# Kernel tuning notes

Measured on AMD Instinct MI355X. Metric: run time of the kernel, lower is better.

Reference implementation:

```python
import jax, jax.numpy as jnp
import numpy as np

B, D, N = 8, 512, 4096
HEADS, DH = 8, 64
HID = HEADS * DH  # 512
SCALE = DH ** -0.5


def setup_inputs() -> dict:
    key = jax.random.key(0)
    k0, k1, k2, k3 = jax.random.split(key, 4)
    x = jax.random.normal(k0, (B, D, N), dtype=jnp.float32)
    w_qkv = jax.random.normal(k1, (3 * HID, D), dtype=jnp.float32) * 0.02
    w_out = jax.random.normal(k2, (D, HID), dtype=jnp.float32) * 0.02
    b_out = jax.random.normal(k3, (D,), dtype=jnp.float32) * 0.02
    g = jnp.ones((1, D, 1), dtype=jnp.float32)
    return {"x": x, "w_qkv": w_qkv, "w_out": w_out, "b_out": b_out, "g": g}


def reference(x, w_qkv, w_out, b_out, g):
    # 1x1 Conv1d (no bias) == channel matmul: [b, 3*HID, n]
    qkv = jnp.einsum('od,bdn->bon', w_qkv, x)
    q, k, v = jnp.split(qkv, 3, axis=1)
    # b (h c) n -> b h c n
    q = q.reshape(B, HEADS, DH, N)
    k = k.reshape(B, HEADS, DH, N)
    v = v.reshape(B, HEADS, DH, N)
    q = jax.nn.softmax(q, axis=2) * SCALE  # softmax over feature dim d
    k = jax.nn.softmax(k, axis=3)          # softmax over sequence dim n
    context = jnp.einsum('bhdn,bhen->bhde', k, v)   # [b,h,d,e]
    out = jnp.einsum('bhde,bhdn->bhen', context, q)  # [b,h,e,n]
    out = out.reshape(B, HID, N)
    # 1x1 Conv1d with bias
    y = jnp.einsum('oh,bhn->bon', w_out, out) + b_out[None, :, None]
    # RMSNorm: F.normalize(y, dim=1) * g * sqrt(D)
    norm = jnp.sqrt(jnp.sum(y * y, axis=1, keepdims=True))
    y = y / jnp.maximum(norm, 1e-12) * g * jnp.asarray(D, y.dtype) ** 0.5
    return y
```

## Files before the change

### kernel.cpp

```cpp
#include <hip/hip_runtime.h>
#include <math.h>

#define B 8
#define D 512
#define N 4096
#define HEADS 8
#define DH 64
#define HID 512
#define O3 1536
#define KDIM 512
#define SCALE 0.125f
#define SQRT_D 22.62741699796952f

typedef __attribute__((ext_vector_type(4))) float f32x4;
typedef __attribute__((ext_vector_type(8))) short bf16x8;

static __device__ __forceinline__ unsigned short f2bf(float f) {
    unsigned int u = __float_as_uint(f);
    unsigned int r = (u + 0x7fffu + ((u >> 16) & 1u)) >> 16;
    return (unsigned short)r;
}

static __device__ __forceinline__ float bf2f(unsigned short u) {
    return __uint_as_float((unsigned int)u << 16);
}

static __device__ __forceinline__ void gload_lds16(const void* g, void* l) {
    __builtin_amdgcn_global_load_lds(
        (const __attribute__((address_space(1))) unsigned int*)g,
        (__attribute__((address_space(3))) unsigned int*)l, 16, 0, 0);
}

__global__ __launch_bounds__(256) void cvt_w(const float* __restrict__ w,
                                             unsigned short* __restrict__ wb) {
    int i = (blockIdx.x * 256 + threadIdx.x) * 4;
    float4 v = *(const float4*)(w + i);
    __align__(8) unsigned short o[4] = {f2bf(v.x), f2bf(v.y), f2bf(v.z), f2bf(v.w)};
    *(uint2*)(wb + i) = *(const uint2*)o;
}

__global__ __launch_bounds__(256) void transpose_x(const float* __restrict__ x,
                                                   unsigned short* __restrict__ xT) {
    __shared__ float tile[64][65];
    const int n0 = blockIdx.x * 64, d0 = blockIdx.y * 64, b = blockIdx.z;
    const float* xb = x + (size_t)b * D * N;
    unsigned short* xTb = xT + (size_t)b * N * KDIM;
    const int t = threadIdx.x;
    const int r = t >> 4, c4 = (t & 15) * 4;
#pragma unroll
    for (int i = 0; i < 4; ++i) {
        int row = r + i * 16;
        float4 v = *(const float4*)(xb + (size_t)(d0 + row) * N + n0 + c4);
        tile[row][c4 + 0] = v.x;
        tile[row][c4 + 1] = v.y;
        tile[row][c4 + 2] = v.z;
        tile[row][c4 + 3] = v.w;
    }
    __syncthreads();
#pragma unroll
    for (int pass = 0; pass < 2; ++pass) {
        int orow = (t >> 3) + pass * 32;
        int oc = (t & 7) * 8;
        __align__(16) unsigned short o[8];
#pragma unroll
        for (int e = 0; e < 8; ++e) o[e] = f2bf(tile[oc + e][orow]);
        *(uint4*)(xTb + (size_t)(n0 + orow) * KDIM + d0 + oc) = *(const uint4*)o;
    }
}

#define STAGE_AB(A_PTR, BT_PTR, BUFOFF, KOFF)                                      \
    _Pragma("unroll") for (int i = 0; i < 4; ++i)                                  \
        gload_lds16(A_PTR + (size_t)(row0 + prow[i]) * KDIM + (KOFF) + coff[i],    \
                    (char*)As + (BUFOFF) + i * 4096 + t * 16);                     \
    _Pragma("unroll") for (int i = 0; i < 4; ++i)                                  \
        gload_lds16(BT_PTR + (size_t)(col0 + prow[i]) * KDIM + (KOFF) + coff[i],   \
                    (char*)Bs + (BUFOFF) + i * 4096 + t * 16);

#define GEMM_CORE_DB(A_PTR, BT_PTR, ACC)                                           \
    __shared__ __align__(16) unsigned short As[2 * 128 * 64];                      \
    __shared__ __align__(16) unsigned short Bs[2 * 128 * 64];                      \
    const int t = threadIdx.x;                                                     \
    const int lane = t & 63;                                                       \
    const int wid = t >> 6;                                                        \
    const int wm = wid >> 1, wn = wid & 1;                                         \
    int prow[4], coff[4];                                                          \
    _Pragma("unroll") for (int i = 0; i < 4; ++i) {                                \
        int p = i * 4096 + t * 16;                                                 \
        int pr = p >> 7;                                                           \
        int pc = (p >> 4) & 7;                                                     \
        prow[i] = pr;                                                              \
        coff[i] = (pc ^ (pr & 7)) * 8;                                             \
    }                                                                              \
    int aoff[4][2], boff[4][2];                                                    \
    _Pragma("unroll") for (int m = 0; m < 4; ++m) {                                \
        int arow = wm * 64 + m * 16 + (lane & 15);                                 \
        int brow = wn * 64 + m * 16 + (lane & 15);                                 \
        _Pragma("unroll") for (int s = 0; s < 2; ++s) {                            \
            int chunk = s * 4 + (lane >> 4);                                       \
            aoff[m][s] = arow * 128 + ((chunk ^ (arow & 7)) << 4);                 \
            boff[m][s] = brow * 128 + ((chunk ^ (brow & 7)) << 4);                 \
        }                                                                          \
    }                                                                              \
    f32x4 ACC[4][4] = {};                                                          \
    { STAGE_AB(A_PTR, BT_PTR, 0, 0) }                                              \
    for (int kt = 0; kt < 8; ++kt) {                                               \
        if (kt < 7) {                                                              \
            STAGE_AB(A_PTR, BT_PTR, ((kt + 1) & 1) * 16384, (kt + 1) * 64)         \
            asm volatile("s_waitcnt vmcnt(8)" ::: "memory");                       \
        } else {                                                                   \
            asm volatile("s_waitcnt vmcnt(0)" ::: "memory");                       \
        }                                                                          \
        __builtin_amdgcn_s_barrier();                                              \
        const int bo = (kt & 1) * 16384;                                           \
        bf16x8 af[4][2], bfr[4][2];                                                \
        _Pragma("unroll") for (int m = 0; m < 4; ++m)                              \
            _Pragma("unroll") for (int s = 0; s < 2; ++s) {                        \
                af[m][s] = *(const bf16x8*)((const char*)As + bo + aoff[m][s]);    \
                bfr[m][s] = *(const bf16x8*)((const char*)Bs + bo + boff[m][s]);   \
            }                                                                      \
        asm volatile("s_waitcnt lgkmcnt(0)" ::: "memory");                         \
        __builtin_amdgcn_sched_barrier(0);                                         \
        __builtin_amdgcn_s_barrier();                                              \
        _Pragma("unroll") for (int s = 0; s < 2; ++s)                              \
            _Pragma("unroll") for (int m = 0; m < 4; ++m)                          \
                _Pragma("unroll") for (int n = 0; n < 4; ++n)                      \
                    ACC[m][n] = __builtin_amdgcn_mfma_f32_16x16x32_bf16(           \
                        af[m][s], bfr[n][s], ACC[m][n], 0, 0, 0);                  \
    }

__global__ __launch_bounds__(256) void gemm_qkv(const unsigned short* __restrict__ Aw,
                                                const unsigned short* __restrict__ BTall,
                                                unsigned short* __restrict__ qT,
                                                unsigned short* __restrict__ kvall) {
    const int b = blockIdx.z;
    const unsigned short* A = Aw;
    const unsigned short* BT = BTall + (size_t)b * N * KDIM;
    const int row0 = blockIdx.y * 128;
    const int col0 = blockIdx.x * 128;
    GEMM_CORE_DB(A, BT, acc)

    if (blockIdx.y < 4) {
        const int h = blockIdx.y * 2 + wm;
        const int g = lane >> 4;
#pragma unroll
        for (int nf = 0; nf < 4; ++nf) {
            float mx = -1e30f;
#pragma unroll
            for (int m = 0; m < 4; ++m)
#pragma unroll
                for (int r = 0; r < 4; ++r) mx = fmaxf(mx, acc[m][nf][r]);
            mx = fmaxf(mx, __shfl_xor(mx, 16));
            mx = fmaxf(mx, __shfl_xor(mx, 32));
            float e[16];
            float s = 0.f;
#pragma unroll
            for (int m = 0; m < 4; ++m)
#pragma unroll
                for (int r = 0; r < 4; ++r) {
                    e[m * 4 + r] = __expf(acc[m][nf][r] - mx);
                    s += e[m * 4 + r];
                }
            s += __shfl_xor(s, 16);
            s += __shfl_xor(s, 32);
            float rs = SCALE / s;
            int n = col0 + wn * 64 + nf * 16 + (lane & 15);
            unsigned short* dst = qT + ((size_t)b * N + n) * KDIM + h * 64 + g * 4;
#pragma unroll
            for (int m = 0; m < 4; ++m) {
                __align__(8) unsigned short o4[4] = {
                    f2bf(e[m * 4 + 0] * rs), f2bf(e[m * 4 + 1] * rs),
                    f2bf(e[m * 4 + 2] * rs), f2bf(e[m * 4 + 3] * rs)};
                *(uint2*)(dst + m * 16) = *(const uint2*)o4;
            }
        }
    } else {
        unsigned short* C = kvall + (size_t)b * 1024 * N;
        const int rbase = row0 - 512;
#pragma unroll
        for (int m = 0; m < 4; ++m) {
            int row_b = rbase + wm * 64 + m * 16 + (lane >> 4) * 4;
#pragma unroll
            for (int n = 0; n < 4; ++n) {
                int col = col0 + wn * 64 + n * 16 + (lane & 15);
#pragma unroll
                for (int r = 0; r < 4; ++r)
                    C[(size_t)(row_b + r) * N + col] = f2bf(acc[m][n][r]);
            }
        }
    }
}

__global__ __launch_bounds__(256) void context_mfma3(const unsigned short* __restrict__ kvb,
                                                     float* __restrict__ ctx,
                                                     float* __restrict__ ksum) {
    const int ch = blockIdx.x, h = blockIdx.y, b = blockIdx.z;
    const int K0 = ch * 512;
    const unsigned short* kbase = kvb + ((size_t)b * 1024 + h * DH) * (size_t)N + K0;
    const unsigned short* vbase = kvb + ((size_t)b * 1024 + 512 + h * DH) * (size_t)N + K0;

    __shared__ __align__(16) unsigned short Ks[64 * 64];
    __shared__ __align__(16) unsigned short Vs[64 * 64];

    const int t = threadIdx.x;
    const int lane = t & 63;
    const int wv = t >> 6;

    const int kr = t >> 2;
    const int kc = (t & 3) * 16;
    const int kchunk0 = kc >> 3;
    const int kdst0 = kr * 128 + (((kchunk0 + 0) ^ (kr & 7)) << 4);
    const int kdst1 = kr * 128 + (((kchunk0 + 1) ^ (kr & 7)) << 4);

    int vrow[2], vcoff[2];
#pragma unroll
    for (int i = 0; i < 2; ++i) {
        int p = i * 4096 + t * 16;
        int pr = p >> 7;
        int pc = (p >> 4) & 7;
        vrow[i] = pr;
        vcoff[i] = (pc ^ (pr & 7)) * 8;
    }

    const int ar = wv * 16 + (lane & 15);
    int aoff[2], boff[4][2];
#pragma unroll
    for (int s = 0; s < 2; ++s) {
        int chunk = s * 4 + (lane >> 4);
        aoff[s] = ar * 128 + ((chunk ^ (ar & 7)) << 4);
#pragma unroll
        for (int nf = 0; nf < 4; ++nf) {
            int br = nf * 16 + (lane & 15);
            boff[nf][s] = br * 128 + ((chunk ^ (br & 7)) << 4);
        }
    }

    bf16x8 ones;
#pragma unroll
    for (int j = 0; j < 8; ++j) ones[j] = (short)0x3F80;

    f32x4 acc[4] = {};
    f32x4 accs = {};

    for (int k0 = 0; k0 < 512; k0 += 64) {
#pragma unroll
        for (int i = 0; i < 2; ++i)
            gload_lds16(vbase + (size_t)vrow[i] * N + k0 + vcoff[i],
                        (char*)Vs + i * 4096 + t * 16);
        __align__(16) unsigned short raw[16];
        *(uint4*)raw = *(const uint4*)(kbase + (size_t)kr * N + k0 + kc);
        *(uint4*)(raw + 8) = *(const uint4*)(kbase + (size_t)kr * N + k0 + kc + 8);
        __align__(16) unsigned short o[16];
#pragma unroll
        for (int j = 0; j < 16; ++j) o[j] = f2bf(__expf(bf2f(raw[j])));
        *(uint4*)((char*)Ks + kdst0) = *(const uint4*)o;
        *(uint4*)((char*)Ks + kdst1) = *(const uint4*)(o + 8);
        __syncthreads();

        bf16x8 av[2], bv[4][2];
#pragma unroll
        for (int s = 0; s < 2; ++s) {
            av[s] = *(const bf16x8*)((const char*)Ks + aoff[s]);
#pragma unroll
            for (int nf = 0; nf < 4; ++nf)
                bv[nf][s] = *(const bf16x8*)((const char*)Vs + boff[nf][s]);
        }
#pragma unroll
        for (int s = 0; s < 2; ++s) {
#pragma unroll
            for (int nf = 0; nf < 4; ++nf)
                acc[nf] = __builtin_amdgcn_mfma_f32_16x16x32_bf16(av[s], bv[nf][s], acc[nf], 0, 0, 0);
            accs = __builtin_amdgcn_mfma_f32_16x16x32_bf16(av[s], ones, accs, 0, 0, 0);
        }
        __syncthreads();
    }

    float* cbase = ctx + ((size_t)(b * HEADS + h)) * DH * DH;
    const int drow = wv * 16 + (lane >> 4) * 4;
#pragma unroll
    for (int nf = 0; nf < 4; ++nf) {
        int e = nf * 16 + (lane & 15);
#pragma unroll
        for (int rr = 0; rr < 4; ++rr)
            atomicAdd(&cbase[(drow + rr) * DH + e], acc[nf][rr]);
    }
    if ((lane & 15) == 0) {
#pragma unroll
        for (int rr = 0; rr < 4; ++rr)
            atomicAdd(&ksum[b * 512 + h * DH + drow + rr], accs[rr]);
    }
}

__global__ __launch_bounds__(256) void fold_wout3(const float* __restrict__ w_out,
                                                  const float* __restrict__ ctx,
                                                  const float* __restrict__ ksum,
                                                  unsigned short* __restrict__ w2) {
    const int ot = blockIdx.x, h = blockIdx.y, b = blockIdx.z;
    __shared__ __align__(16) unsigned short As[128 * 64];
    __shared__ __align__(16) unsigned short Bs[64 * 64];
    const int t = threadIdx.x;
    const int lane = t & 63;
    const int wv = t >> 6;

#pragma unroll
    for (int i = 0; i < 8; ++i) {
        int lin = t + i * 256;
        int r = lin >> 4;
        int c4 = (lin & 15) * 4;
        float4 v = *(const float4*)(w_out + (size_t)(ot * 128 + r) * HID + h * 64 + c4);
        __align__(8) unsigned short o4[4] = {f2bf(v.x), f2bf(v.y), f2bf(v.z), f2bf(v.w)};
        int chunk = c4 >> 3;
        int off = (c4 & 7) * 2;
        *(uint2*)((char*)As + r * 128 + ((chunk ^ (r & 7)) << 4) + off) = *(const uint2*)o4;
    }
    const float* cb = ctx + ((size_t)(b * HEADS + h)) * DH * DH;
    const float* ks = ksum + b * 512 + h * 64;
#pragma unroll
    for (int i = 0; i < 4; ++i) {
        int lin = t + i * 256;
        int r = lin >> 4;
        int c4 = (lin & 15) * 4;
        float inv = 1.0f / ks[r];
        float4 v = *(const float4*)(cb + (size_t)r * DH + c4);
        __align__(8) unsigned short o4[4] = {f2bf(v.x * inv), f2bf(v.y * inv),
                                             f2bf(v.z * inv), f2bf(v.w * inv)};
        int chunk = c4 >> 3;
        int off = (c4 & 7) * 2;
        *(uint2*)((char*)Bs + r * 128 + ((chunk ^ (r & 7)) << 4) + off) = *(const uint2*)o4;
    }
    __syncthreads();

    f32x4 acc[2][4] = {};
#pragma unroll
    for (int s = 0; s < 2; ++s) {
        int chunk = s * 4 + (lane >> 4);
        bf16x8 bf[4];
#pragma unroll
        for (int nf = 0; nf < 4; ++nf) {
            int brow = nf * 16 + (lane & 15);
            bf[nf] = *(const bf16x8*)((const char*)Bs + brow * 128 + ((chunk ^ (brow & 7)) << 4));
        }
#pragma unroll
        for (int mm = 0; mm < 2; ++mm) {
            int arow = (wv * 2 + mm) * 16 + (lane & 15);
            bf16x8 a = *(const bf16x8*)((const char*)As + arow * 128 + ((chunk ^ (arow & 7)) << 4));
#pragma unroll
            for (int nf = 0; nf < 4; ++nf)
                acc[mm][nf] = __builtin_amdgcn_mfma_f32_16x16x32_bf16(a, bf[nf], acc[mm][nf], 0, 0, 0);
        }
    }

#pragma unroll
    for (int mm = 0; mm < 2; ++mm) {
        int o_base = ot * 128 + (wv * 2 + mm) * 16 + (lane >> 4) * 4;
#pragma unroll
        for (int nf = 0; nf < 4; ++nf) {
            int d = nf * 16 + (lane & 15);
#pragma unroll
            for (int rr = 0; rr < 4; ++rr)
                w2[((size_t)(b * D) + o_base + rr) * D + h * 64 + d] = f2bf(acc[mm][nf][rr]);
        }
    }
}

__global__ __launch_bounds__(256) void gemm_y(const unsigned short* __restrict__ w2all,
                                              const unsigned short* __restrict__ qTall,
                                              const float* __restrict__ bias,
                                              float* __restrict__ yall,
                                              float* __restrict__ colsum) {
    const int b = blockIdx.z;
    const unsigned short* A = w2all + (size_t)b * D * D;
    const unsigned short* BT = qTall + (size_t)b * N * KDIM;
    float* y = yall + (size_t)b * D * N;
    const int row0 = blockIdx.y * 128;
    const int col0 = blockIdx.x * 128;
    GEMM_CORE_DB(A, BT, acc)

    float csum[4] = {0.f, 0.f, 0.f, 0.f};
#pragma unroll
    for (int m = 0; m < 4; ++m) {
        int row_b = row0 + wm * 64 + m * 16 + (lane >> 4) * 4;
#pragma unroll
        for (int r = 0; r < 4; ++r) {
            float bv = bias[row_b + r];
#pragma unroll
            for (int n = 0; n < 4; ++n) {
                int col = col0 + wn * 64 + n * 16 + (lane & 15);
                float e = acc[m][n][r] + bv;
                y[(size_t)(row_b + r) * N + col] = e;
                csum[n] += e * e;
            }
        }
    }
#pragma unroll
    for (int n = 0; n < 4; ++n) {
        csum[n] += __shfl_xor(csum[n], 16);
        csum[n] += __shfl_xor(csum[n], 32);
    }
    if (lane < 16) {
#pragma unroll
        for (int n = 0; n < 4; ++n) {
            int col = col0 + wn * 64 + n * 16 + lane;
            atomicAdd(&colsum[b * N + col], csum[n]);
        }
    }
}

__global__ __launch_bounds__(256) void colprep(float* __restrict__ cs) {
    int i = blockIdx.x * 256 + threadIdx.x;
    float v = cs[i];
    cs[i] = SQRT_D / fmaxf(sqrtf(v), 1e-12f);
}

__global__ __launch_bounds__(256) void rmsnorm4(float4* __restrict__ y,
                                                const float4* __restrict__ rinv,
                                                const float* __restrict__ g) {
    const size_t total = (size_t)B * D * N / 4;
    for (size_t i = blockIdx.x * 256 + threadIdx.x; i < total; i += 524288) {
        int b = (int)(i >> 19);
        int rem = (int)(i & 524287);
        int o = rem >> 10;
        int n4 = rem & 1023;
        float4 v = y[i];
        float4 rv = rinv[b * 1024 + n4];
        float go = g[o];
        v.x *= rv.x * go;
        v.y *= rv.y * go;
        v.z *= rv.z * go;
        v.w *= rv.w * go;
        y[i] = v;
    }
}

extern "C" void kernel_launch(void* const* d_in, const int* in_sizes, int n_in,
                              void* d_out, int out_size, void* d_ws, size_t ws_size,
                              hipStream_t stream) {
    const float* x = (const float*)d_in[0];
    const float* w_qkv = (const float*)d_in[1];
    const float* w_out = (const float*)d_in[2];
    const float* b_out = (const float*)d_in[3];
    const float* g = (const float*)d_in[4];
    float* out = (float*)d_out;

    unsigned short* kvb = (unsigned short*)d_ws;
    float* ctx = (float*)(kvb + (size_t)B * 1024 * N);
    float* ksum = ctx + (size_t)B * HEADS * DH * DH;
    float* colsum = ksum + B * 512;
    unsigned short* w2 = (unsigned short*)(colsum + B * N);
    unsigned short* wqb = w2 + (size_t)B * D * D;
    unsigned short* xT = wqb + (size_t)O3 * KDIM;
    unsigned short* qT = xT + (size_t)B * N * KDIM;

    hipMemsetAsync(ctx, 0,
                   ((size_t)B * HEADS * DH * DH + B * 512 + B * N) * sizeof(float), stream);

    cvt_w<<<dim3(O3 * KDIM / 1024), 256, 0, stream>>>(w_qkv, wqb);
    transpose_x<<<dim3(N / 64, D / 64, B), 256, 0, stream>>>(x, xT);

    gemm_qkv<<<dim3(N / 128, O3 / 128, B), 256, 0, stream>>>(wqb, xT, qT, kvb);

    context_mfma3<<<dim3(8, HEADS, B), 256, 0, stream>>>(kvb, ctx, ksum);
    fold_wout3<<<dim3(4, HEADS, B), 256, 0, stream>>>(w_out, ctx, ksum, w2);

    gemm_y<<<dim3(N / 128, D / 128, B), 256, 0, stream>>>(w2, qT, b_out, out, colsum);

    colprep<<<dim3(B * N / 256), 256, 0, stream>>>(colsum);
    rmsnorm4<<<dim3(2048), 256, 0, stream>>>((float4*)out, (const float4*)colsum, g);
}
```

Measured before the change: 166.1 us.

## Load GEMM A fragments directly from global into registers, double-buffered

The A operand (weights) is no longer staged through shared memory. Each lane now loads its MFMA fragments straight from global memory into two register buffers, one prefetched a step ahead, while B keeps its LDS double buffer. This removes half of the LDS traffic and LDS footprint and some ds_read work per k-step. The cost is uncoalesced 16-byte global loads per lane with duplication across waves, more VGPRs for the double-buffered fragments, and a fully unrolled k loop.

```diff
diff --git a/kernel.cpp b/kernel.cpp
--- a/kernel.cpp
+++ b/kernel.cpp
@@ -68,16 +68,17 @@
     }
 }
 
-#define STAGE_AB(A_PTR, BT_PTR, BUFOFF, KOFF)                                      \
-    _Pragma("unroll") for (int i = 0; i < 4; ++i)                                  \
-        gload_lds16(A_PTR + (size_t)(row0 + prow[i]) * KDIM + (KOFF) + coff[i],    \
-                    (char*)As + (BUFOFF) + i * 4096 + t * 16);                     \
+#define STAGE_B(BT_PTR, BUFOFF, KOFF)                                              \
     _Pragma("unroll") for (int i = 0; i < 4; ++i)                                  \
         gload_lds16(BT_PTR + (size_t)(col0 + prow[i]) * KDIM + (KOFF) + coff[i],   \
                     (char*)Bs + (BUFOFF) + i * 4096 + t * 16);
 
-#define GEMM_CORE_DB(A_PTR, BT_PTR, ACC)                                           \
-    __shared__ __align__(16) unsigned short As[2 * 128 * 64];                      \
+#define LOAD_A(DST, KOFF)                                                          \
+    _Pragma("unroll") for (int m = 0; m < 4; ++m)                                  \
+        _Pragma("unroll") for (int s = 0; s < 2; ++s)                              \
+            DST[m][s] = *(const bf16x8*)(arow_[m] + (KOFF) + s * 32);
+
+#define GEMM_CORE_AG(A_PTR, BT_PTR, ACC)                                           \
     __shared__ __align__(16) unsigned short Bs[2 * 128 * 64];                      \
     const int t = threadIdx.x;                                                     \
     const int lane = t & 63;                                                       \
@@ -91,33 +92,40 @@
         prow[i] = pr;                                                              \
         coff[i] = (pc ^ (pr & 7)) * 8;                                             \
     }                                                                              \
-    int aoff[4][2], boff[4][2];                                                    \
-    _Pragma("unroll") for (int m = 0; m < 4; ++m) {                                \
-        int arow = wm * 64 + m * 16 + (lane & 15);                                 \
-        int brow = wn * 64 + m * 16 + (lane & 15);                                 \
+    int boff[4][2];                                                                \
+    _Pragma("unroll") for (int n = 0; n < 4; ++n) {                                \
+        int brow = wn * 64 + n * 16 + (lane & 15);                                 \
         _Pragma("unroll") for (int s = 0; s < 2; ++s) {                            \
             int chunk = s * 4 + (lane >> 4);                                       \
-            aoff[m][s] = arow * 128 + ((chunk ^ (arow & 7)) << 4);                 \
-            boff[m][s] = brow * 128 + ((chunk ^ (brow & 7)) << 4);                 \
+            boff[n][s] = brow * 128 + ((chunk ^ (brow & 7)) << 4);                 \
         }                                                                          \
     }                                                                              \
+    const unsigned short* arow_[4];                                                \
+    _Pragma("unroll") for (int m = 0; m < 4; ++m)                                  \
+        arow_[m] = A_PTR + (size_t)(row0 + wm * 64 + m * 16 + (lane & 15)) * KDIM  \
+                   + 8 * (lane >> 4);                                              \
     f32x4 ACC[4][4] = {};                                                          \
-    { STAGE_AB(A_PTR, BT_PTR, 0, 0) }                                              \
-    for (int kt = 0; kt < 8; ++kt) {                                               \
+    bf16x8 afA[4][2], afB[4][2];                                                   \
+    { STAGE_B(BT_PTR, 0, 0) }                                                      \
+    LOAD_A(afA, 0)                                                                 \
+    _Pragma("unroll") for (int kt = 0; kt < 8; ++kt) {                             \
         if (kt < 7) {                                                              \
-            STAGE_AB(A_PTR, BT_PTR, ((kt + 1) & 1) * 16384, (kt + 1) * 64)         \
-            asm volatile("s_waitcnt vmcnt(8)" ::: "memory");                       \
+            STAGE_B(BT_PTR, ((kt + 1) & 1) * 16384, (kt + 1) * 64)                 \
+            if ((kt & 1) == 0) {                                                   \
+                LOAD_A(afB, (kt + 1) * 64)                                         \
+            } else {                                                               \
+                LOAD_A(afA, (kt + 1) * 64)                                         \
+            }                                                                      \
+            asm volatile("s_waitcnt vmcnt(12)" ::: "memory");                      \
         } else {                                                                   \
             asm volatile("s_waitcnt vmcnt(0)" ::: "memory");                       \
         }                                                                          \
         __builtin_amdgcn_s_barrier();                                              \
         const int bo = (kt & 1) * 16384;                                           \
-        bf16x8 af[4][2], bfr[4][2];                                                \
-        _Pragma("unroll") for (int m = 0; m < 4; ++m)                              \
-            _Pragma("unroll") for (int s = 0; s < 2; ++s) {                        \
-                af[m][s] = *(const bf16x8*)((const char*)As + bo + aoff[m][s]);    \
-                bfr[m][s] = *(const bf16x8*)((const char*)Bs + bo + boff[m][s]);   \
-            }                                                                      \
+        bf16x8 bfr[4][2];                                                          \
+        _Pragma("unroll") for (int n = 0; n < 4; ++n)                              \
+            _Pragma("unroll") for (int s = 0; s < 2; ++s)                          \
+                bfr[n][s] = *(const bf16x8*)((const char*)Bs + bo + boff[n][s]);   \
         asm volatile("s_waitcnt lgkmcnt(0)" ::: "memory");                         \
         __builtin_amdgcn_sched_barrier(0);                                         \
         __builtin_amdgcn_s_barrier();                                              \
@@ -125,7 +133,7 @@
             _Pragma("unroll") for (int m = 0; m < 4; ++m)                          \
                 _Pragma("unroll") for (int n = 0; n < 4; ++n)                      \
                     ACC[m][n] = __builtin_amdgcn_mfma_f32_16x16x32_bf16(           \
-                        af[m][s], bfr[n][s], ACC[m][n], 0, 0, 0);                  \
+                        ((kt & 1) ? afB : afA)[m][s], bfr[n][s], ACC[m][n], 0, 0, 0); \
     }
 
 __global__ __launch_bounds__(256) void gemm_qkv(const unsigned short* __restrict__ Aw,
@@ -137,7 +145,7 @@
     const unsigned short* BT = BTall + (size_t)b * N * KDIM;
     const int row0 = blockIdx.y * 128;
     const int col0 = blockIdx.x * 128;
-    GEMM_CORE_DB(A, BT, acc)
+    GEMM_CORE_AG(A, BT, acc)
 
     if (blockIdx.y < 4) {
         const int h = blockIdx.y * 2 + wm;
@@ -373,7 +381,7 @@
     float* y = yall + (size_t)b * D * N;
     const int row0 = blockIdx.y * 128;
     const int col0 = blockIdx.x * 128;
-    GEMM_CORE_DB(A, BT, acc)
+    GEMM_CORE_AG(A, BT, acc)
 
     float csum[4] = {0.f, 0.f, 0.f, 0.f};
 #pragma unroll
```

Result: slower. 233.8 us (+40.7%).

## Use 256x256 GEMM tiles with 8 waves and interleaved staged loads

Applied to the files above, without the earlier changes.

Both projection GEMMs move from 128x128 tiles with 4 waves to 256x256 tiles with 8 waves and 128KB of double-buffered LDS. The main loop now interleaves next-tile global-to-LDS loads with four phases of fragment loads and MFMAs, and raises wave priority around the MFMA blocks. The larger tiles are meant to improve operand reuse and hide memory latency. In exchange there are fewer blocks (grid of 16x2x8 for gemm_y), heavier register and LDS pressure that may limit occupancy, and reworked epilogue indexing.

```diff
diff --git a/kernel.cpp b/kernel.cpp
--- a/kernel.cpp
+++ b/kernel.cpp
@@ -68,123 +68,135 @@
     }
 }
 
-#define STAGE_AB(A_PTR, BT_PTR, BUFOFF, KOFF)                                      \
-    _Pragma("unroll") for (int i = 0; i < 4; ++i)                                  \
-        gload_lds16(A_PTR + (size_t)(row0 + prow[i]) * KDIM + (KOFF) + coff[i],    \
-                    (char*)As + (BUFOFF) + i * 4096 + t * 16);                     \
-    _Pragma("unroll") for (int i = 0; i < 4; ++i)                                  \
-        gload_lds16(BT_PTR + (size_t)(col0 + prow[i]) * KDIM + (KOFF) + coff[i],   \
-                    (char*)Bs + (BUFOFF) + i * 4096 + t * 16);
-
-#define GEMM_CORE_DB(A_PTR, BT_PTR, ACC)                                           \
-    __shared__ __align__(16) unsigned short As[2 * 128 * 64];                      \
-    __shared__ __align__(16) unsigned short Bs[2 * 128 * 64];                      \
+#define STAGE_H(PTR, REGION, TILE0, KT, H)                                         \
+    _Pragma("unroll") for (int sub = 0; sub < 2; ++sub)                            \
+        gload_lds16(PTR + (size_t)((TILE0) + (H) * 128 + spr[sub]) * KDIM          \
+                        + (KT) * 64 + scoff[sub],                                  \
+                    lds + (REGION) + ((KT) & 1) * 32768 + (H) * 16384              \
+                        + sub * 8192 + t * 16);
+
+#define PHASE_A(MG, KS)                                                            \
+    _Pragma("unroll") for (int j = 0; j < 4; ++j)                                  \
+        afr[j] = *(const bf16x8*)(lds + rbuf + arb + ((MG) * 4 + j) * 2048 + xa[KS]);
+
+#define PHASE_B(KS)                                                                \
+    _Pragma("unroll") for (int nf = 0; nf < 4; ++nf)                               \
+        bfr[nf] = *(const bf16x8*)(lds + 65536 + rbuf + brb + nf * 2048 + xa[KS]);
+
+#define PHASE_MMA(MG)                                                              \
+    asm volatile("s_waitcnt lgkmcnt(0)" ::: "memory");                             \
+    __builtin_amdgcn_sched_barrier(0);                                             \
+    __builtin_amdgcn_s_setprio(1);                                                 \
+    _Pragma("unroll") for (int j = 0; j < 4; ++j)                                  \
+        _Pragma("unroll") for (int nf = 0; nf < 4; ++nf)                           \
+            acc[(MG) * 4 + j][nf] = __builtin_amdgcn_mfma_f32_16x16x32_bf16(       \
+                afr[j], bfr[nf], acc[(MG) * 4 + j][nf], 0, 0, 0);                  \
+    __builtin_amdgcn_s_setprio(0);
+
+#define GEMM256_CORE(A_PTR, BT_PTR)                                                \
+    __shared__ __align__(16) char lds[131072];                                     \
     const int t = threadIdx.x;                                                     \
     const int lane = t & 63;                                                       \
     const int wid = t >> 6;                                                        \
-    const int wm = wid >> 1, wn = wid & 1;                                         \
-    int prow[4], coff[4];                                                          \
-    _Pragma("unroll") for (int i = 0; i < 4; ++i) {                                \
-        int p = i * 4096 + t * 16;                                                 \
-        int pr = p >> 7;                                                           \
-        int pc = (p >> 4) & 7;                                                     \
-        prow[i] = pr;                                                              \
-        coff[i] = (pc ^ (pr & 7)) * 8;                                             \
+    const int wm = wid >> 2, wn = wid & 3;                                         \
+    int spr[2], scoff[2];                                                          \
+    _Pragma("unroll") for (int sub = 0; sub < 2; ++sub) {                          \
+        int p = sub * 8192 + t * 16;                                               \
+        spr[sub] = p >> 7;                                                         \
+        int spc = (p >> 4) & 7;                                                    \
+        scoff[sub] = (spc ^ (spr[sub] & 7)) * 8;                                   \
     }                                                                              \
-    int aoff[4][2], boff[4][2];                                                    \
-    _Pragma("unroll") for (int m = 0; m < 4; ++m) {                                \
-        int arow = wm * 64 + m * 16 + (lane & 15);                                 \
-        int brow = wn * 64 + m * 16 + (lane & 15);                                 \
-        _Pragma("unroll") for (int s = 0; s < 2; ++s) {                            \
-            int chunk = s * 4 + (lane >> 4);                                       \
-            aoff[m][s] = arow * 128 + ((chunk ^ (arow & 7)) << 4);                 \
-            boff[m][s] = brow * 128 + ((chunk ^ (brow & 7)) << 4);                 \
-        }                                                                          \
-    }                                                                              \
-    f32x4 ACC[4][4] = {};                                                          \
-    { STAGE_AB(A_PTR, BT_PTR, 0, 0) }                                              \
+    int xa[2];                                                                     \
+    _Pragma("unroll") for (int ks = 0; ks < 2; ++ks)                               \
+        xa[ks] = ((ks * 4 + (lane >> 4)) ^ (lane & 7)) << 4;                       \
+    const int arb = (wm * 128 + (lane & 15)) * 128;                                \
+    const int brb = (wn * 64 + (lane & 15)) * 128;                                 \
+    f32x4 acc[8][4] = {};                                                          \
+    bf16x8 afr[4], bfr[4];                                                         \
+    STAGE_H(A_PTR, 0, row0, 0, 0)                                                  \
+    STAGE_H(A_PTR, 0, row0, 0, 1)                                                  \
+    STAGE_H(BT_PTR, 65536, col0, 0, 0)                                             \
+    STAGE_H(BT_PTR, 65536, col0, 0, 1)                                             \
     for (int kt = 0; kt < 8; ++kt) {                                               \
+        const int rbuf = (kt & 1) * 32768;                                         \
+        __builtin_amdgcn_s_barrier();                                              \
         if (kt < 7) {                                                              \
-            STAGE_AB(A_PTR, BT_PTR, ((kt + 1) & 1) * 16384, (kt + 1) * 64)         \
-            asm volatile("s_waitcnt vmcnt(8)" ::: "memory");                       \
+            STAGE_H(A_PTR, 0, row0, kt + 1, 0)                                     \
+            asm volatile("s_waitcnt vmcnt(2)" ::: "memory");                       \
         } else {                                                                   \
             asm volatile("s_waitcnt vmcnt(0)" ::: "memory");                       \
         }                                                                          \
         __builtin_amdgcn_s_barrier();                                              \
-        const int bo = (kt & 1) * 16384;                                           \
-        bf16x8 af[4][2], bfr[4][2];                                                \
-        _Pragma("unroll") for (int m = 0; m < 4; ++m)                              \
-            _Pragma("unroll") for (int s = 0; s < 2; ++s) {                        \
-                af[m][s] = *(const bf16x8*)((const char*)As + bo + aoff[m][s]);    \
-                bfr[m][s] = *(const bf16x8*)((const char*)Bs + bo + boff[m][s]);   \
-            }                                                                      \
-        asm volatile("s_waitcnt lgkmcnt(0)" ::: "memory");                         \
         __builtin_amdgcn_sched_barrier(0);                                         \
-        __builtin_amdgcn_s_barrier();                                              \
-        _Pragma("unroll") for (int s = 0; s < 2; ++s)                              \
-            _Pragma("unroll") for (int m = 0; m < 4; ++m)                          \
-                _Pragma("unroll") for (int n = 0; n < 4; ++n)                      \
-                    ACC[m][n] = __builtin_amdgcn_mfma_f32_16x16x32_bf16(           \
-                        af[m][s], bfr[n][s], ACC[m][n], 0, 0, 0);                  \
-    }
-
-__global__ __launch_bounds__(256) void gemm_qkv(const unsigned short* __restrict__ Aw,
-                                                const unsigned short* __restrict__ BTall,
-                                                unsigned short* __restrict__ qT,
-                                                unsigned short* __restrict__ kvall) {
+        PHASE_A(0, 0) PHASE_B(0) PHASE_MMA(0)                                      \
+        if (kt < 7) { STAGE_H(A_PTR, 0, row0, kt + 1, 1) }                         \
+        PHASE_A(1, 0) PHASE_MMA(1)                                                 \
+        if (kt < 7) { STAGE_H(BT_PTR, 65536, col0, kt + 1, 0) }                    \
+        PHASE_A(0, 1) PHASE_B(1) PHASE_MMA(0)                                      \
+        if (kt < 7) { STAGE_H(BT_PTR, 65536, col0, kt + 1, 1) }                    \
+        PHASE_A(1, 1) PHASE_MMA(1)                                                 \
+    }
+
+__global__ __launch_bounds__(512, 2) void gemm_qkv(const unsigned short* __restrict__ Aw,
+                                                   const unsigned short* __restrict__ BTall,
+                                                   unsigned short* __restrict__ qT,
+                                                   unsigned short* __restrict__ kvall) {
     const int b = blockIdx.z;
     const unsigned short* A = Aw;
     const unsigned short* BT = BTall + (size_t)b * N * KDIM;
-    const int row0 = blockIdx.y * 128;
-    const int col0 = blockIdx.x * 128;
-    GEMM_CORE_DB(A, BT, acc)
-
-    if (blockIdx.y < 4) {
-        const int h = blockIdx.y * 2 + wm;
-        const int g = lane >> 4;
-#pragma unroll
-        for (int nf = 0; nf < 4; ++nf) {
-            float mx = -1e30f;
-#pragma unroll
-            for (int m = 0; m < 4; ++m)
-#pragma unroll
-                for (int r = 0; r < 4; ++r) mx = fmaxf(mx, acc[m][nf][r]);
-            mx = fmaxf(mx, __shfl_xor(mx, 16));
-            mx = fmaxf(mx, __shfl_xor(mx, 32));
-            float e[16];
-            float s = 0.f;
-#pragma unroll
-            for (int m = 0; m < 4; ++m)
-#pragma unroll
-                for (int r = 0; r < 4; ++r) {
-                    e[m * 4 + r] = __expf(acc[m][nf][r] - mx);
-                    s += e[m * 4 + r];
+    const int row0 = blockIdx.y * 256;
+    const int col0 = blockIdx.x * 256;
+    GEMM256_CORE(A, BT)
+
+    const int g = lane >> 4;
+    if (blockIdx.y < 2) {
+#pragma unroll
+        for (int g2 = 0; g2 < 2; ++g2) {
+            const int h = blockIdx.y * 4 + wm * 2 + g2;
+#pragma unroll
+            for (int nf = 0; nf < 4; ++nf) {
+                float mx = -1e30f;
+#pragma unroll
+                for (int j = 0; j < 4; ++j)
+#pragma unroll
+                    for (int r = 0; r < 4; ++r) mx = fmaxf(mx, acc[g2 * 4 + j][nf][r]);
+                mx = fmaxf(mx, __shfl_xor(mx, 16));
+                mx = fmaxf(mx, __shfl_xor(mx, 32));
+                float e[16];
+                float s = 0.f;
+#pragma unroll
+                for (int j = 0; j < 4; ++j)
+#pragma unroll
+                    for (int r = 0; r < 4; ++r) {
+                        e[j * 4 + r] = __expf(acc[g2 * 4 + j][nf][r] - mx);
+                        s += e[j * 4 + r];
+                    }
+                s += __shfl_xor(s, 16);
+                s += __shfl_xor(s, 32);
+                float rs = SCALE / s;
+                int n = col0 + wn * 64 + nf * 16 + (lane & 15);
+                unsigned short* dst = qT + ((size_t)b * N + n) * KDIM + h * 64 + g * 4;
+#pragma unroll
+                for (int j = 0; j < 4; ++j) {
+                    __align__(8) unsigned short o4[4] = {
+                        f2bf(e[j * 4 + 0] * rs), f2bf(e[j * 4 + 1] * rs),
+                        f2bf(e[j * 4 + 2] * rs), f2bf(e[j * 4 + 3] * rs)};
+                    *(uint2*)(dst + j * 16) = *(const uint2*)o4;
                 }
-            s += __shfl_xor(s, 16);
-            s += __shfl_xor(s, 32);
-            float rs = SCALE / s;
-            int n = col0 + wn * 64 + nf * 16 + (lane & 15);
-            unsigned short* dst = qT + ((size_t)b * N + n) * KDIM + h * 64 + g * 4;
-#pragma unroll
-            for (int m = 0; m < 4; ++m) {
-                __align__(8) unsigned short o4[4] = {
-                    f2bf(e[m * 4 + 0] * rs), f2bf(e[m * 4 + 1] * rs),
-                    f2bf(e[m * 4 + 2] * rs), f2bf(e[m * 4 + 3] * rs)};
-                *(uint2*)(dst + m * 16) = *(const uint2*)o4;
             }
         }
     } else {
         unsigned short* C = kvall + (size_t)b * 1024 * N;
-        const int rbase = row0 - 512;
-#pragma unroll
-        for (int m = 0; m < 4; ++m) {
-            int row_b = rbase + wm * 64 + m * 16 + (lane >> 4) * 4;
-#pragma unroll
-            for (int n = 0; n < 4; ++n) {
-                int col = col0 + wn * 64 + n * 16 + (lane & 15);
+        const int rbase = row0 - 512 + wm * 128;
+#pragma unroll
+        for (int mf = 0; mf < 8; ++mf) {
+            int row_b = rbase + mf * 16 + g * 4;
+#pragma unroll
+            for (int nf = 0; nf < 4; ++nf) {
+                int col = col0 + wn * 64 + nf * 16 + (lane & 15);
 #pragma unroll
                 for (int r = 0; r < 4; ++r)
-                    C[(size_t)(row_b + r) * N + col] = f2bf(acc[m][n][r]);
+                    C[(size_t)(row_b + r) * N + col] = f2bf(acc[mf][nf][r]);
             }
         }
     }
@@ -362,45 +374,46 @@
     }
 }
 
-__global__ __launch_bounds__(256) void gemm_y(const unsigned short* __restrict__ w2all,
-                                              const unsigned short* __restrict__ qTall,
-                                              const float* __restrict__ bias,
-                                              float* __restrict__ yall,
-                                              float* __restrict__ colsum) {
+__global__ __launch_bounds__(512, 2) void gemm_y(const unsigned short* __restrict__ w2all,
+                                                 const unsigned short* __restrict__ qTall,
+                                                 const float* __restrict__ bias,
+                                                 float* __restrict__ yall,
+                                                 float* __restrict__ colsum) {
     const int b = blockIdx.z;
     const unsigned short* A = w2all + (size_t)b * D * D;
     const unsigned short* BT = qTall + (size_t)b * N * KDIM;
     float* y = yall + (size_t)b * D * N;
-    const int row0 = blockIdx.y * 128;
-    const int col0 = blockIdx.x * 128;
-    GEMM_CORE_DB(A, BT, acc)
-
+    const int row0 = blockIdx.y * 256;
+    const int col0 = blockIdx.x * 256;
+    GEMM256_CORE(A, BT)
+
+    const int g = lane >> 4;
     float csum[4] = {0.f, 0.f, 0.f, 0.f};
 #pragma unroll
-    for (int m = 0; m < 4; ++m) {
-        int row_b = row0 + wm * 64 + m * 16 + (lane >> 4) * 4;
+    for (int mf = 0; mf < 8; ++mf) {
+        int row_b = row0 + wm * 128 + mf * 16 + g * 4;
 #pragma unroll
         for (int r = 0; r < 4; ++r) {
             float bv = bias[row_b + r];
 #pragma unroll
-            for (int n = 0; n < 4; ++n) {
-                int col = col0 + wn * 64 + n * 16 + (lane & 15);
-                float e = acc[m][n][r] + bv;
+            for (int nf = 0; nf < 4; ++nf) {
+                int col = col0 + wn * 64 + nf * 16 + (lane & 15);
+                float e = acc[mf][nf][r] + bv;
                 y[(size_t)(row_b + r) * N + col] = e;
-                csum[n] += e * e;
+                csum[nf] += e * e;
             }
         }
     }
 #pragma unroll
-    for (int n = 0; n < 4; ++n) {
-        csum[n] += __shfl_xor(csum[n], 16);
-        csum[n] += __shfl_xor(csum[n], 32);
-    }
-    if (lane < 16) {
-#pragma unroll
-        for (int n = 0; n < 4; ++n) {
-            int col = col0 + wn * 64 + n * 16 + lane;
-            atomicAdd(&colsum[b * N + col], csum[n]);
+    for (int nf = 0; nf < 4; ++nf) {
+        csum[nf] += __shfl_xor(csum[nf], 16);
+        csum[nf] += __shfl_xor(csum[nf], 32);
+    }
+    if ((lane & 48) == 0) {
+#pragma unroll
+        for (int nf = 0; nf < 4; ++nf) {
+            int col = col0 + wn * 64 + nf * 16 + (lane & 15);
+            atomicAdd(&colsum[b * N + col], csum[nf]);
         }
     }
 }
@@ -456,12 +469,12 @@
     cvt_w<<<dim3(O3 * KDIM / 1024), 256, 0, stream>>>(w_qkv, wqb);
     transpose_x<<<dim3(N / 64, D / 64, B), 256, 0, stream>>>(x, xT);
 
-    gemm_qkv<<<dim3(N / 128, O3 / 128, B), 256, 0, stream>>>(wqb, xT, qT, kvb);
+    gemm_qkv<<<dim3(N / 256, O3 / 256, B), 512, 0, stream>>>(wqb, xT, qT, kvb);
 
     context_mfma3<<<dim3(8, HEADS, B), 256, 0, stream>>>(kvb, ctx, ksum);
     fold_wout3<<<dim3(4, HEADS, B), 256, 0, stream>>>(w_out, ctx, ksum, w2);
 
-    gemm_y<<<dim3(N / 128, D / 128, B), 256, 0, stream>>>(w2, qT, b_out, out, colsum);
+    gemm_y<<<dim3(N / 256, D / 256, B), 512, 0, stream>>>(w2, qT, b_out, out, colsum);
 
     colprep<<<dim3(B * N / 256), 256, 0, stream>>>(colsum);
     rmsnorm4<<<dim3(2048), 256, 0, stream>>>((float4*)out, (const float4*)colsum, g);
```

Result: faster. 162.1 us (-2.5%).
